# Performance work log

Measured on AMD Instinct MI355X. Metric: run time of the kernel, lower is better.

The kernel has to match this reference:

```python
import jax, jax.numpy as jnp
import numpy as np

NUM_HEADS = 2
HIDDEN_DIM = 128  # == node_dim
HEAD_DIM = 64     # node_dim // num_heads
NEG_SLOPE = 0.2
N_NODES = 25000
N_EDGES = 400000
NODE_DIM = 128
EDGE_DIM = 64


def setup_inputs() -> dict:
    key = jax.random.key(0)
    ks = jax.random.split(key, 16)
    s = 0.05
    return {
        "node_features": jax.random.normal(ks[0], (N_NODES, NODE_DIM), jnp.float32),
        "edge_features": jax.random.normal(ks[1], (N_EDGES, EDGE_DIM), jnp.float32),
        "edge_index": jax.random.randint(ks[2], (2, N_EDGES), 0, N_NODES, jnp.int32),
        "ni_W": jax.random.normal(ks[3], (NODE_DIM, NUM_HEADS * HIDDEN_DIM), jnp.float32) * s,
        "ni_b": jax.random.normal(ks[4], (NUM_HEADS * HIDDEN_DIM,), jnp.float32) * s,
        "nj_W": jax.random.normal(ks[5], (NODE_DIM, NUM_HEADS * HIDDEN_DIM), jnp.float32) * s,
        "nj_b": jax.random.normal(ks[6], (NUM_HEADS * HIDDEN_DIM,), jnp.float32) * s,
        "e_W": jax.random.normal(ks[7], (EDGE_DIM, NUM_HEADS * HIDDEN_DIM), jnp.float32) * s,
        "e_b": jax.random.normal(ks[8], (NUM_HEADS * HIDDEN_DIM,), jnp.float32) * s,
        "attn_proj": jax.random.normal(ks[9], (NUM_HEADS, HIDDEN_DIM), jnp.float32),
        "msg_W": jax.random.normal(ks[10], (NODE_DIM + EDGE_DIM, NODE_DIM), jnp.float32) * s,
        "msg_b": jax.random.normal(ks[11], (NODE_DIM,), jnp.float32) * s,
        "out_W": jax.random.normal(ks[12], (NODE_DIM, NODE_DIM), jnp.float32) * s,
        "out_b": jax.random.normal(ks[13], (NODE_DIM,), jnp.float32) * s,
    }


def _scatter_softmax(logits, seg, num_segments):
    # logits: [E, H], seg: [E] -> per-destination-node softmax over incident edges
    seg_max = jax.ops.segment_max(logits, seg, num_segments=num_segments)  # [N, H]
    ex = jnp.exp(logits - seg_max[seg])
    denom = jax.ops.segment_sum(ex, seg, num_segments=num_segments)  # [N, H]
    return ex / denom[seg]


def reference(node_features, edge_features, edge_index, ni_W, ni_b, nj_W, nj_b,
              e_W, e_b, attn_proj, msg_W, msg_b, out_W, out_b):
    n_nodes = node_features.shape[0]
    dst = edge_index[0]  # aggregation index (indices()[0])
    src = edge_index[1]
    ni = node_features[dst]  # [E, D]
    nj = node_features[src]  # [E, D]

    hidden = ni @ ni_W + ni_b + nj @ nj_W + nj_b + edge_features @ e_W + e_b  # [E, H*hid]
    hidden = jnp.where(hidden >= 0, hidden, NEG_SLOPE * hidden)  # LeakyReLU
    hidden = hidden.reshape(-1, NUM_HEADS, HIDDEN_DIM)

    attn_logits = jnp.einsum('ehd,hd->eh', hidden, attn_proj)  # [E, H]
    attn = _scatter_softmax(attn_logits, dst, n_nodes)  # [E, H]

    messages = jnp.concatenate((nj, edge_features), axis=-1) @ msg_W + msg_b  # [E, D]
    messages = messages.reshape(-1, NUM_HEADS, HEAD_DIM) * attn[:, :, None]
    agg = jax.ops.segment_sum(messages, dst, num_segments=n_nodes)  # [N, H, head]
    agg = agg.reshape(n_nodes, NUM_HEADS * HEAD_DIM)
    return agg @ out_W + out_b
```

## Files before the change

### kernel.cpp

```cpp
#include <hip/hip_runtime.h>

#define NEG 0.2f
typedef unsigned short u16;
typedef __bf16 bf8 __attribute__((ext_vector_type(8)));
typedef float f4 __attribute__((ext_vector_type(4)));
typedef u16 u16x8 __attribute__((ext_vector_type(8)));

#define OFF_P16   0ull
#define SZ_P16    (25000ull*256ull)
#define OFF_PM16  (OFF_P16 + SZ_P16)
#define SZ_PM16   (25000ull*64ull)
#define OFF_BCF   (OFF_PM16 + SZ_PM16)
#define SZ_BCF    40960ull
#define OFF_BTOT  (OFF_BCF + SZ_BCF)
#define SZ_BTOT   256ull
#define OFF_LOG   (OFF_BTOT + SZ_BTOT)
#define SZ_LOG    (2ull*400000ull)
#define OFF_MAX   (OFF_LOG + SZ_LOG)
#define SZ_MAX    (2ull*25000ull)
#define OFF_DEN   (OFF_MAX + SZ_MAX)
#define SZ_DEN    (2ull*25000ull)
#define OFF_AGG   (OFF_DEN + SZ_DEN)
#define SZ_AGG    (25000ull*128ull)
#define OFF_CNT   (OFF_AGG + SZ_AGG)
#define SZ_CNT    25000ull
#define OFF_CUR   (OFF_CNT + SZ_CNT)
#define SZ_CUR    25000ull
#define OFF_PERM  (OFF_CUR + SZ_CUR)
#define SZ_PERM   400000ull
#define OFF_DST   (OFF_PERM + SZ_PERM)
#define SZ_DST    400000ull
#define OFF_SRC   (OFF_DST + SZ_DST)
#define SZ_SRC    400000ull
#define OFF_EWF   (OFF_SRC + SZ_SRC)
#define SZ_EWF    8192ull
#define OFF_MWF   (OFF_EWF + SZ_EWF)
#define SZ_MWF    4096ull

__device__ __forceinline__ unsigned fkey(float f) {
    unsigned u = __float_as_uint(f);
    return (u & 0x80000000u) ? ~u : (u | 0x80000000u);
}
__device__ __forceinline__ float keyf(unsigned k) {
    unsigned u = (k & 0x80000000u) ? (k & 0x7fffffffu) : ~k;
    return __uint_as_float(u);
}
__device__ __forceinline__ u16 f2b(float f) {
    unsigned u = __float_as_uint(f);
    return (u16)((u + 0x7FFFu + ((u >> 16) & 1u)) >> 16);
}
__device__ __forceinline__ float b2f(u16 v) {
    return __uint_as_float(((unsigned)v) << 16);
}
__device__ __forceinline__ bf8 pack8(float4 a, float4 b) {
    union { u16 u[8]; bf8 v; } x;
    x.u[0] = f2b(a.x); x.u[1] = f2b(a.y); x.u[2] = f2b(a.z); x.u[3] = f2b(a.w);
    x.u[4] = f2b(b.x); x.u[5] = f2b(b.y); x.u[6] = f2b(b.z); x.u[7] = f2b(b.w);
    return x.v;
}

__global__ void k_prep(const float* __restrict__ niW, const float* __restrict__ njW,
                       const float* __restrict__ msgW, const float* __restrict__ eW,
                       const float* __restrict__ nib, const float* __restrict__ njb,
                       const float* __restrict__ eb,
                       u16* __restrict__ bcf, float* __restrict__ btot,
                       u16* __restrict__ ewfrag, u16* __restrict__ msgfrag) {
    int idx = blockIdx.x * 256 + threadIdx.x;
    if (idx < 81920) {
        int fi = idx >> 9;
        int ln = (idx >> 3) & 63, i = idx & 7;
        int cb = fi >> 2, s = fi & 3;
        int k = s * 32 + ((ln >> 4) << 3) + i;
        int col = cb * 16 + (ln & 15);
        float v = (col < 256) ? niW[k * 256 + col]
                : (col < 512) ? njW[k * 256 + (col - 256)]
                              : msgW[k * 128 + (col - 512)];
        bcf[idx] = f2b(v);
    }
    if (idx < 16384) {
        int c = idx >> 10, s = (idx >> 9) & 1, ln = (idx >> 3) & 63, i = idx & 7;
        int k = s * 32 + ((ln >> 4) << 3) + i;
        int col = c * 16 + (ln & 15);
        ewfrag[idx] = f2b(eW[k * 256 + col]);
    }
    if (idx < 8192) {
        int c = idx >> 10, s = (idx >> 9) & 1, ln = (idx >> 3) & 63, i = idx & 7;
        int k = s * 32 + ((ln >> 4) << 3) + i;
        int col = c * 16 + (ln & 15);
        msgfrag[idx] = f2b(msgW[(128 + k) * 128 + col]);
    }
    if (idx < 256) btot[idx] = nib[idx] + njb[idx] + eb[idx];
}

__device__ __forceinline__ void gemm_tile(const float* Al, int astride, int acol0,
                                          const float* Bl, int trow, int tcol,
                                          float acc[4][8]) {
    for (int k4 = 0; k4 < 64; k4 += 4) {
        float ar[4][4];
#pragma unroll
        for (int r = 0; r < 4; ++r)
            *(float4*)ar[r] = *(const float4*)&Al[(trow * 4 + r) * astride + acol0 + k4];
#pragma unroll
        for (int kk = 0; kk < 4; ++kk) {
            float4 b0 = *(const float4*)&Bl[(k4 + kk) * 128 + tcol * 8];
            float4 b1 = *(const float4*)&Bl[(k4 + kk) * 128 + tcol * 8 + 4];
            float bv[8] = {b0.x, b0.y, b0.z, b0.w, b1.x, b1.y, b1.z, b1.w};
#pragma unroll
            for (int r = 0; r < 4; ++r) {
                float av = ar[r][kk];
#pragma unroll
                for (int j = 0; j < 8; ++j) acc[r][j] = fmaf(av, bv[j], acc[r][j]);
            }
        }
    }
}

__global__ __launch_bounds__(256) void k_node_pre(const float* __restrict__ nf,
                                                  const u16* __restrict__ bcf,
                                                  u16* __restrict__ pre16,
                                                  u16* __restrict__ premsg16) {
    int t = threadIdx.x, w = t >> 6, l = t & 63;
    int n0 = blockIdx.x * 64 + w * 16;
    int rsel = l & 15, kb = l >> 4;
    int nA = n0 + rsel;
    size_t nAc = (nA < 25000) ? (size_t)nA : 24999;
    const float* ap = &nf[nAc * 128 + kb * 8];
    bf8 a[4];
#pragma unroll
    for (int s = 0; s < 4; ++s) {
        float4 x = *(const float4*)&ap[s * 32];
        float4 y = *(const float4*)&ap[s * 32 + 4];
        a[s] = pack8(x, y);
    }
    int nC = n0 + kb * 4;
#pragma unroll 4
    for (int cb = 0; cb < 40; ++cb) {
        f4 acc = {0.f, 0.f, 0.f, 0.f};
#pragma unroll
        for (int s = 0; s < 4; ++s) {
            bf8 b = *(const bf8*)&bcf[(size_t)((cb * 4 + s) * 64 + l) * 8];
            acc = __builtin_amdgcn_mfma_f32_16x16x32_bf16(a[s], b, acc, 0, 0, 0);
        }
#pragma unroll
        for (int r = 0; r < 4; ++r) {
            int nn = nC + r;
            if (nn < 25000) {
                if (cb < 32) pre16[(size_t)nn * 512 + cb * 16 + rsel] = f2b(acc[r]);
                else premsg16[(size_t)nn * 128 + (cb - 32) * 16 + rsel] = f2b(acc[r]);
            }
        }
    }
}

__global__ void k_hist(const int* __restrict__ eidx, int* __restrict__ count) {
    int e = blockIdx.x * 256 + threadIdx.x;
    if (e < 400000) atomicAdd(&count[eidx[e]], 1);
}

__global__ __launch_bounds__(1024) void k_scan(const int* __restrict__ count,
                                               int* __restrict__ cursor) {
    __shared__ int sums[1024];
    int t = threadIdx.x;
    int base = t * 25;
    int v[25];
    int local = 0;
#pragma unroll
    for (int i = 0; i < 25; ++i) {
        int idx = base + i;
        int c = (idx < 25000) ? count[idx] : 0;
        v[i] = local;
        local += c;
    }
    sums[t] = local;
    __syncthreads();
    for (int off = 1; off < 1024; off <<= 1) {
        int x = (t >= off) ? sums[t - off] : 0;
        __syncthreads();
        sums[t] += x;
        __syncthreads();
    }
    int prefix = (t == 0) ? 0 : sums[t - 1];
#pragma unroll
    for (int i = 0; i < 25; ++i) {
        int idx = base + i;
        if (idx < 25000) cursor[idx] = prefix + v[i];
    }
}

__global__ void k_scatter(const int* __restrict__ eidx, int* __restrict__ cursor,
                          int* __restrict__ perm, int* __restrict__ dsts,
                          int* __restrict__ srcs) {
    int e = blockIdx.x * 256 + threadIdx.x;
    if (e < 400000) {
        int d = eidx[e];
        int p = atomicAdd(&cursor[d], 1);
        perm[p] = e;
        dsts[p] = d;
        srcs[p] = eidx[400000 + e];
    }
}

__global__ __launch_bounds__(256) void k_edge_logits(
        const float* __restrict__ ef, const int* __restrict__ perm,
        const int* __restrict__ dsts, const int* __restrict__ srcs,
        const u16* __restrict__ ewfrag, const u16* __restrict__ pre16,
        const float* __restrict__ btot, const float* __restrict__ aproj,
        float* __restrict__ logits_s, unsigned* __restrict__ maxkey) {
    __shared__ int eperm[64], dstl[64], srcl[64];
    int t = threadIdx.x;
    int w = t >> 6, l = t & 63;
    int p0 = blockIdx.x * 64;
    int row = l & 15, kb = l >> 4;

    if (t < 64) {
        eperm[t] = perm[p0 + t];
        dstl[t] = dsts[p0 + t];
        srcl[t] = srcs[p0 + t];
    }
    __syncthreads();

    int ea = eperm[w * 16 + row];
    const float* ap = &ef[(size_t)ea * 64 + kb * 8];
    float4 a00 = *(const float4*)ap;
    float4 a01 = *(const float4*)(ap + 4);
    float4 a10 = *(const float4*)(ap + 32);
    float4 a11 = *(const float4*)(ap + 36);
    bf8 a0 = pack8(a00, a01), a1 = pack8(a10, a11);

    int ed[4], es[4];
#pragma unroll
    for (int r = 0; r < 4; ++r) {
        int i4 = w * 16 + kb * 4 + r;
        ed[r] = dstl[i4];
        es[r] = srcl[i4];
    }

    float part0[4] = {0.f, 0.f, 0.f, 0.f}, part1[4] = {0.f, 0.f, 0.f, 0.f};
#pragma unroll
    for (int c = 0; c < 16; ++c) {
        bf8 b0 = *(const bf8*)&ewfrag[(size_t)((c * 2 + 0) * 64 + l) * 8];
        bf8 b1 = *(const bf8*)&ewfrag[(size_t)((c * 2 + 1) * 64 + l) * 8];
        f4 acc = {0.f, 0.f, 0.f, 0.f};
        acc = __builtin_amdgcn_mfma_f32_16x16x32_bf16(a0, b0, acc, 0, 0, 0);
        acc = __builtin_amdgcn_mfma_f32_16x16x32_bf16(a1, b1, acc, 0, 0, 0);
        int col = c * 16 + row;
        float bt = btot[col], apj = aproj[col];
#pragma unroll
        for (int r = 0; r < 4; ++r) {
            float pi = b2f(pre16[(size_t)ed[r] * 512 + col]);
            float pj = b2f(pre16[(size_t)es[r] * 512 + 256 + col]);
            float hid = acc[r] + pi + pj + bt;
            hid = hid >= 0.f ? hid : NEG * hid;
            if (c < 8) part0[r] = fmaf(hid, apj, part0[r]);
            else       part1[r] = fmaf(hid, apj, part1[r]);
        }
    }
#pragma unroll
    for (int m = 1; m < 16; m <<= 1) {
#pragma unroll
        for (int r = 0; r < 4; ++r) {
            part0[r] += __shfl_xor(part0[r], m);
            part1[r] += __shfl_xor(part1[r], m);
        }
    }
    if (row == 0) {
#pragma unroll
        for (int r = 0; r < 4; ++r) {
            int p = p0 + w * 16 + kb * 4 + r;
            logits_s[(size_t)p * 2 + 0] = part0[r];
            logits_s[(size_t)p * 2 + 1] = part1[r];
            atomicMax(&maxkey[ed[r] * 2 + 0], fkey(part0[r]));
            atomicMax(&maxkey[ed[r] * 2 + 1], fkey(part1[r]));
        }
    }
}

__global__ void k_soft(const int* __restrict__ dsts, float* __restrict__ logits_s,
                       const unsigned* __restrict__ maxkey, float* __restrict__ denom) {
    int idx = blockIdx.x * 256 + threadIdx.x;
    if (idx >= 800000) return;
    int p = idx >> 1, h = idx & 1;
    int d = dsts[p];
    float m = keyf(maxkey[d * 2 + h]);
    float ex = __expf(logits_s[idx] - m);
    logits_s[idx] = ex;
    atomicAdd(&denom[d * 2 + h], ex);
}

__global__ __launch_bounds__(256) void k_messages(
        const float* __restrict__ ef, const int* __restrict__ perm,
        const int* __restrict__ dsts, const int* __restrict__ srcs,
        const u16* __restrict__ msgfrag, const u16* __restrict__ premsg16,
        const float* __restrict__ exs, const float* __restrict__ denom,
        float* __restrict__ agg) {
    __shared__ float Msg[64 * 132];
    __shared__ int dstl[64], srcl[64], eperm[64];
    __shared__ float attl[64][2];
    int t = threadIdx.x;
    int w = t >> 6, l = t & 63;
    int p0 = blockIdx.x * 64;
    int row = l & 15, kb = l >> 4;

    if (t < 64) {
        int p = p0 + t;
        eperm[t] = perm[p];
        int d = dsts[p];
        dstl[t] = d;
        srcl[t] = srcs[p];
        attl[t][0] = exs[(size_t)p * 2 + 0] / denom[d * 2 + 0];
        attl[t][1] = exs[(size_t)p * 2 + 1] / denom[d * 2 + 1];
    }
    __syncthreads();

    int ea = eperm[w * 16 + row];
    const float* apr = &ef[(size_t)ea * 64 + kb * 8];
    float4 a00 = *(const float4*)apr;
    float4 a01 = *(const float4*)(apr + 4);
    float4 a10 = *(const float4*)(apr + 32);
    float4 a11 = *(const float4*)(apr + 36);
    bf8 a0 = pack8(a00, a01), a1 = pack8(a10, a11);

    int esr[4];
    float at0[4], at1[4];
#pragma unroll
    for (int r = 0; r < 4; ++r) {
        int i4 = w * 16 + kb * 4 + r;
        esr[r] = srcl[i4];
        at0[r] = attl[i4][0];
        at1[r] = attl[i4][1];
    }

#pragma unroll
    for (int c = 0; c < 8; ++c) {
        bf8 b0 = *(const bf8*)&msgfrag[(size_t)((c * 2 + 0) * 64 + l) * 8];
        bf8 b1 = *(const bf8*)&msgfrag[(size_t)((c * 2 + 1) * 64 + l) * 8];
        f4 acc = {0.f, 0.f, 0.f, 0.f};
        acc = __builtin_amdgcn_mfma_f32_16x16x32_bf16(a0, b0, acc, 0, 0, 0);
        acc = __builtin_amdgcn_mfma_f32_16x16x32_bf16(a1, b1, acc, 0, 0, 0);
        int col = c * 16 + row;
#pragma unroll
        for (int r = 0; r < 4; ++r) {
            float m = acc[r] + b2f(premsg16[(size_t)esr[r] * 128 + col]);
            float wm = ((c < 4) ? at0[r] : at1[r]) * m;
            Msg[(w * 16 + kb * 4 + r) * 132 + col] = wm;
        }
    }
    __syncthreads();

    int c = t & 127, half = t >> 7;
    int r0 = half * 32, r1 = r0 + 32;
    int cur = dstl[r0];
    float sum = 0.f;
    for (int r = r0; r < r1; ++r) {
        int d = dstl[r];
        if (d != cur) {
            atomicAdd(&agg[(size_t)cur * 128 + c], sum);
            sum = 0.f;
            cur = d;
        }
        sum += Msg[r * 132 + c];
    }
    atomicAdd(&agg[(size_t)cur * 128 + c], sum);
}

__global__ __launch_bounds__(256) void k_out(
        const float* __restrict__ agg, const int* __restrict__ count,
        const float* __restrict__ msgb, const float* __restrict__ outW,
        const float* __restrict__ outb, float* __restrict__ out) {
    __shared__ float Al[64 * 128];
    __shared__ float Bl[64 * 128];
    int t = threadIdx.x, n0 = blockIdx.x * 64;
    int trow = t >> 4, tcol = t & 15;
#pragma unroll
    for (int q = 0; q < 8; ++q) {
        int g = t + 256 * q;
        int i = g >> 5, k4 = (g & 31) * 4;
        int n = n0 + i;
        float4 v = make_float4(0.f, 0.f, 0.f, 0.f);
        if (n < 25000) {
            v = *(const float4*)&agg[(size_t)n * 128 + k4];
            if (count[n] > 0) {
                float4 mb = *(const float4*)&msgb[k4];
                v.x += mb.x; v.y += mb.y; v.z += mb.z; v.w += mb.w;
            }
        }
        *(float4*)&Al[i * 128 + k4] = v;
    }
    float acc[4][8] = {};
    for (int kh = 0; kh < 2; ++kh) {
        __syncthreads();
#pragma unroll
        for (int q = 0; q < 8; ++q) {
            int g = t + 256 * q;
            int k = g >> 5, c4 = (g & 31) * 4;
            *(float4*)&Bl[k * 128 + c4] = *(const float4*)&outW[(kh * 64 + k) * 128 + c4];
        }
        __syncthreads();
        gemm_tile(Al, 128, kh * 64, Bl, trow, tcol, acc);
    }
    float ob[8];
    *(float4*)ob = *(const float4*)&outb[tcol * 8];
    *(float4*)(ob + 4) = *(const float4*)&outb[tcol * 8 + 4];
#pragma unroll
    for (int r = 0; r < 4; ++r) {
        int n = n0 + trow * 4 + r;
        if (n < 25000) {
            *(float4*)&out[(size_t)n * 128 + tcol * 8] =
                make_float4(acc[r][0] + ob[0], acc[r][1] + ob[1], acc[r][2] + ob[2], acc[r][3] + ob[3]);
            *(float4*)&out[(size_t)n * 128 + tcol * 8 + 4] =
                make_float4(acc[r][4] + ob[4], acc[r][5] + ob[5], acc[r][6] + ob[6], acc[r][7] + ob[7]);
        }
    }
}

extern "C" void kernel_launch(void* const* d_in, const int* in_sizes, int n_in,
                              void* d_out, int out_size, void* d_ws, size_t ws_size,
                              hipStream_t stream) {
    const float* nf    = (const float*)d_in[0];
    const float* ef    = (const float*)d_in[1];
    const int*   eidx  = (const int*)d_in[2];
    const float* niW   = (const float*)d_in[3];
    const float* nib   = (const float*)d_in[4];
    const float* njW   = (const float*)d_in[5];
    const float* njb   = (const float*)d_in[6];
    const float* eW    = (const float*)d_in[7];
    const float* eb    = (const float*)d_in[8];
    const float* aproj = (const float*)d_in[9];
    const float* msgW  = (const float*)d_in[10];
    const float* msgb  = (const float*)d_in[11];
    const float* outW  = (const float*)d_in[12];
    const float* outb  = (const float*)d_in[13];

    float* ws = (float*)d_ws;
    u16*   pre16     = (u16*)(ws + OFF_P16);
    u16*   premsg16  = (u16*)(ws + OFF_PM16);
    u16*   bcf       = (u16*)(ws + OFF_BCF);
    float* btot      = ws + OFF_BTOT;
    float* logits_s  = ws + OFF_LOG;
    unsigned* maxkey = (unsigned*)(ws + OFF_MAX);
    float* denom     = ws + OFF_DEN;
    float* agg       = ws + OFF_AGG;
    int*   count     = (int*)(ws + OFF_CNT);
    int*   cursor    = (int*)(ws + OFF_CUR);
    int*   perm      = (int*)(ws + OFF_PERM);
    int*   dsts      = (int*)(ws + OFF_DST);
    int*   srcs      = (int*)(ws + OFF_SRC);
    u16*   ewfrag    = (u16*)(ws + OFF_EWF);
    u16*   msgfrag   = (u16*)(ws + OFF_MWF);

    hipMemsetAsync(ws + OFF_MAX, 0, (size_t)(SZ_MAX + SZ_DEN + SZ_AGG + SZ_CNT) * 4, stream);

    k_prep<<<320, 256, 0, stream>>>(niW, njW, msgW, eW, nib, njb, eb,
                                    bcf, btot, ewfrag, msgfrag);
    k_node_pre<<<391, 256, 0, stream>>>(nf, bcf, pre16, premsg16);
    k_hist<<<1563, 256, 0, stream>>>(eidx, count);
    k_scan<<<1, 1024, 0, stream>>>(count, cursor);
    k_scatter<<<1563, 256, 0, stream>>>(eidx, cursor, perm, dsts, srcs);
    k_edge_logits<<<6250, 256, 0, stream>>>(ef, perm, dsts, srcs, ewfrag, pre16,
                                            btot, aproj, logits_s, maxkey);
    k_soft<<<3125, 256, 0, stream>>>(dsts, logits_s, maxkey, denom);
    k_messages<<<6250, 256, 0, stream>>>(ef, perm, dsts, srcs, msgfrag, premsg16,
                                         logits_s, denom, agg);
    k_out<<<391, 256, 0, stream>>>(agg, count, msgb, outW, outb, (float*)d_out);
}
```

Measured before the change: 324.3 us.

## Fuse edge logits, softmax and message aggregation; defer normalization to output

Merges the logits, softmax and message kernels into one edge kernel. It computes exp(logit) directly, with no per-destination max subtraction, and scatters exp-weighted messages and denominators with atomics. Division by the denominator moves into the output GEMM load. This removes two kernel launches, the logits buffer round trip, the atomicMax pass and the second read of edge features and indices. In exchange, softmax is no longer max-stabilized, so large logits could overflow in fp32.

```diff
diff --git a/kernel.cpp b/kernel.cpp
--- a/kernel.cpp
+++ b/kernel.cpp
@@ -14,11 +14,7 @@
 #define SZ_BCF    40960ull
 #define OFF_BTOT  (OFF_BCF + SZ_BCF)
 #define SZ_BTOT   256ull
-#define OFF_LOG   (OFF_BTOT + SZ_BTOT)
-#define SZ_LOG    (2ull*400000ull)
-#define OFF_MAX   (OFF_LOG + SZ_LOG)
-#define SZ_MAX    (2ull*25000ull)
-#define OFF_DEN   (OFF_MAX + SZ_MAX)
+#define OFF_DEN   (OFF_BTOT + SZ_BTOT)
 #define SZ_DEN    (2ull*25000ull)
 #define OFF_AGG   (OFF_DEN + SZ_DEN)
 #define SZ_AGG    (25000ull*128ull)
@@ -37,14 +33,6 @@
 #define OFF_MWF   (OFF_EWF + SZ_EWF)
 #define SZ_MWF    4096ull
 
-__device__ __forceinline__ unsigned fkey(float f) {
-    unsigned u = __float_as_uint(f);
-    return (u & 0x80000000u) ? ~u : (u | 0x80000000u);
-}
-__device__ __forceinline__ float keyf(unsigned k) {
-    unsigned u = (k & 0x80000000u) ? (k & 0x7fffffffu) : ~k;
-    return __uint_as_float(u);
-}
 __device__ __forceinline__ u16 f2b(float f) {
     unsigned u = __float_as_uint(f);
     return (u16)((u + 0x7FFFu + ((u >> 16) & 1u)) >> 16);
@@ -200,12 +188,14 @@
     }
 }
 
-__global__ __launch_bounds__(256) void k_edge_logits(
+__global__ __launch_bounds__(256) void k_edge_fused(
         const float* __restrict__ ef, const int* __restrict__ perm,
         const int* __restrict__ dsts, const int* __restrict__ srcs,
-        const u16* __restrict__ ewfrag, const u16* __restrict__ pre16,
+        const u16* __restrict__ ewfrag, const u16* __restrict__ msgfrag,
+        const u16* __restrict__ pre16, const u16* __restrict__ premsg16,
         const float* __restrict__ btot, const float* __restrict__ aproj,
-        float* __restrict__ logits_s, unsigned* __restrict__ maxkey) {
+        float* __restrict__ denom, float* __restrict__ agg) {
+    __shared__ float Msg[64 * 132];
     __shared__ int eperm[64], dstl[64], srcl[64];
     int t = threadIdx.x;
     int w = t >> 6, l = t & 63;
@@ -263,71 +253,18 @@
             part1[r] += __shfl_xor(part1[r], m);
         }
     }
+    float ex0[4], ex1[4];
+#pragma unroll
+    for (int r = 0; r < 4; ++r) {
+        ex0[r] = __expf(part0[r]);
+        ex1[r] = __expf(part1[r]);
+    }
     if (row == 0) {
 #pragma unroll
         for (int r = 0; r < 4; ++r) {
-            int p = p0 + w * 16 + kb * 4 + r;
-            logits_s[(size_t)p * 2 + 0] = part0[r];
-            logits_s[(size_t)p * 2 + 1] = part1[r];
-            atomicMax(&maxkey[ed[r] * 2 + 0], fkey(part0[r]));
-            atomicMax(&maxkey[ed[r] * 2 + 1], fkey(part1[r]));
-        }
-    }
-}
-
-__global__ void k_soft(const int* __restrict__ dsts, float* __restrict__ logits_s,
-                       const unsigned* __restrict__ maxkey, float* __restrict__ denom) {
-    int idx = blockIdx.x * 256 + threadIdx.x;
-    if (idx >= 800000) return;
-    int p = idx >> 1, h = idx & 1;
-    int d = dsts[p];
-    float m = keyf(maxkey[d * 2 + h]);
-    float ex = __expf(logits_s[idx] - m);
-    logits_s[idx] = ex;
-    atomicAdd(&denom[d * 2 + h], ex);
-}
-
-__global__ __launch_bounds__(256) void k_messages(
-        const float* __restrict__ ef, const int* __restrict__ perm,
-        const int* __restrict__ dsts, const int* __restrict__ srcs,
-        const u16* __restrict__ msgfrag, const u16* __restrict__ premsg16,
-        const float* __restrict__ exs, const float* __restrict__ denom,
-        float* __restrict__ agg) {
-    __shared__ float Msg[64 * 132];
-    __shared__ int dstl[64], srcl[64], eperm[64];
-    __shared__ float attl[64][2];
-    int t = threadIdx.x;
-    int w = t >> 6, l = t & 63;
-    int p0 = blockIdx.x * 64;
-    int row = l & 15, kb = l >> 4;
-
-    if (t < 64) {
-        int p = p0 + t;
-        eperm[t] = perm[p];
-        int d = dsts[p];
-        dstl[t] = d;
-        srcl[t] = srcs[p];
-        attl[t][0] = exs[(size_t)p * 2 + 0] / denom[d * 2 + 0];
-        attl[t][1] = exs[(size_t)p * 2 + 1] / denom[d * 2 + 1];
-    }
-    __syncthreads();
-
-    int ea = eperm[w * 16 + row];
-    const float* apr = &ef[(size_t)ea * 64 + kb * 8];
-    float4 a00 = *(const float4*)apr;
-    float4 a01 = *(const float4*)(apr + 4);
-    float4 a10 = *(const float4*)(apr + 32);
-    float4 a11 = *(const float4*)(apr + 36);
-    bf8 a0 = pack8(a00, a01), a1 = pack8(a10, a11);
-
-    int esr[4];
-    float at0[4], at1[4];
-#pragma unroll
-    for (int r = 0; r < 4; ++r) {
-        int i4 = w * 16 + kb * 4 + r;
-        esr[r] = srcl[i4];
-        at0[r] = attl[i4][0];
-        at1[r] = attl[i4][1];
+            atomicAdd(&denom[ed[r] * 2 + 0], ex0[r]);
+            atomicAdd(&denom[ed[r] * 2 + 1], ex1[r]);
+        }
     }
 
 #pragma unroll
@@ -340,9 +277,10 @@
         int col = c * 16 + row;
 #pragma unroll
         for (int r = 0; r < 4; ++r) {
-            float m = acc[r] + b2f(premsg16[(size_t)esr[r] * 128 + col]);
-            float wm = ((c < 4) ? at0[r] : at1[r]) * m;
-            Msg[(w * 16 + kb * 4 + r) * 132 + col] = wm;
+            int i4 = w * 16 + kb * 4 + r;
+            float m = acc[r] + b2f(premsg16[(size_t)es[r] * 128 + col]);
+            float wm = ((c < 4) ? ex0[r] : ex1[r]) * m;
+            Msg[i4 * 132 + col] = wm;
         }
     }
     __syncthreads();
@@ -364,7 +302,8 @@
 }
 
 __global__ __launch_bounds__(256) void k_out(
-        const float* __restrict__ agg, const int* __restrict__ count,
+        const float* __restrict__ agg, const float* __restrict__ denom,
+        const int* __restrict__ count,
         const float* __restrict__ msgb, const float* __restrict__ outW,
         const float* __restrict__ outb, float* __restrict__ out) {
     __shared__ float Al[64 * 128];
@@ -377,12 +316,12 @@
         int i = g >> 5, k4 = (g & 31) * 4;
         int n = n0 + i;
         float4 v = make_float4(0.f, 0.f, 0.f, 0.f);
-        if (n < 25000) {
+        if (n < 25000 && count[n] > 0) {
             v = *(const float4*)&agg[(size_t)n * 128 + k4];
-            if (count[n] > 0) {
-                float4 mb = *(const float4*)&msgb[k4];
-                v.x += mb.x; v.y += mb.y; v.z += mb.z; v.w += mb.w;
-            }
+            float invd = 1.f / denom[n * 2 + (k4 >> 6)];
+            float4 mb = *(const float4*)&msgb[k4];
+            v.x = v.x * invd + mb.x; v.y = v.y * invd + mb.y;
+            v.z = v.z * invd + mb.z; v.w = v.w * invd + mb.w;
         }
         *(float4*)&Al[i * 128 + k4] = v;
     }
@@ -436,8 +375,6 @@
     u16*   premsg16  = (u16*)(ws + OFF_PM16);
     u16*   bcf       = (u16*)(ws + OFF_BCF);
     float* btot      = ws + OFF_BTOT;
-    float* logits_s  = ws + OFF_LOG;
-    unsigned* maxkey = (unsigned*)(ws + OFF_MAX);
     float* denom     = ws + OFF_DEN;
     float* agg       = ws + OFF_AGG;
     int*   count     = (int*)(ws + OFF_CNT);
@@ -448,7 +385,7 @@
     u16*   ewfrag    = (u16*)(ws + OFF_EWF);
     u16*   msgfrag   = (u16*)(ws + OFF_MWF);
 
-    hipMemsetAsync(ws + OFF_MAX, 0, (size_t)(SZ_MAX + SZ_DEN + SZ_AGG + SZ_CNT) * 4, stream);
+    hipMemsetAsync(ws + OFF_DEN, 0, (size_t)(SZ_DEN + SZ_AGG + SZ_CNT) * 4, stream);
 
     k_prep<<<320, 256, 0, stream>>>(niW, njW, msgW, eW, nib, njb, eb,
                                     bcf, btot, ewfrag, msgfrag);
@@ -456,10 +393,7 @@
     k_hist<<<1563, 256, 0, stream>>>(eidx, count);
     k_scan<<<1, 1024, 0, stream>>>(count, cursor);
     k_scatter<<<1563, 256, 0, stream>>>(eidx, cursor, perm, dsts, srcs);
-    k_edge_logits<<<6250, 256, 0, stream>>>(ef, perm, dsts, srcs, ewfrag, pre16,
-                                            btot, aproj, logits_s, maxkey);
-    k_soft<<<3125, 256, 0, stream>>>(dsts, logits_s, maxkey, denom);
-    k_messages<<<6250, 256, 0, stream>>>(ef, perm, dsts, srcs, msgfrag, premsg16,
-                                         logits_s, denom, agg);
-    k_out<<<391, 256, 0, stream>>>(agg, count, msgb, outW, outb, (float*)d_out);
-}
+    k_edge_fused<<<6250, 256, 0, stream>>>(ef, perm, dsts, srcs, ewfrag, msgfrag,
+                                           pre16, premsg16, btot, aproj, denom, agg);
+    k_out<<<391, 256, 0, stream>>>(agg, denom, count, msgb, outW, outb, (float*)d_out);
+}
```

After: 357.6 us. 1.1x slower.
